# Kernel tuning notes

Hardware: AMD Instinct MI355X
Metric: run time of the kernel (lower is better)

The kernel has to match this reference:

```python
import jax, jax.numpy as jnp
from jax import lax
import numpy as np

INPUT_SIZE = 3
RESERVOIR = 2048
OUTPUT_SIZE = 3
SPECTRAL_RADIUS = 0.9
SPARSITY = 0.1
B, T = 16, 2048


def setup_inputs() -> dict:
    key = jax.random.key(0)
    kx, kwin, kw, kmask, kwo, kb = jax.random.split(key, 6)
    x = jax.random.normal(kx, (B, T, INPUT_SIZE), dtype=jnp.float32)
    Win = jax.random.normal(kwin, (RESERVOIR, INPUT_SIZE), dtype=jnp.float32)
    W = jax.random.normal(kw, (RESERVOIR, RESERVOIR), dtype=jnp.float32)
    # spectral-radius rescale (circular law: rho(randn(R,R)) ~ sqrt(R)), then sparsify
    W = W * (SPECTRAL_RADIUS / jnp.sqrt(jnp.float32(RESERVOIR)))
    mask = (jax.random.uniform(kmask, (RESERVOIR, RESERVOIR)) < SPARSITY).astype(jnp.float32)
    W = W * mask
    bound = 1.0 / np.sqrt(RESERVOIR)
    Wout_w = jax.random.uniform(kwo, (OUTPUT_SIZE, RESERVOIR), minval=-bound, maxval=bound, dtype=jnp.float32)
    Wout_b = jax.random.uniform(kb, (OUTPUT_SIZE,), minval=-bound, maxval=bound, dtype=jnp.float32)
    return {"x": x, "Win": Win, "W": W, "Wout_w": Wout_w, "Wout_b": Wout_b}


def reference(x, Win, W, Wout_w, Wout_b):
    Bsz = x.shape[0]
    R = W.shape[0]
    h0 = jnp.zeros((Bsz, R), dtype=x.dtype)

    def step(h, xt):
        h_new = jnp.tanh(xt @ Win.T + h @ W.T)  # [B, R]
        return h_new, h_new

    _, hs = lax.scan(step, h0, jnp.swapaxes(x, 0, 1))  # hs: [T, B, R]
    outs = hs @ Wout_w.T + Wout_b  # [T, B, O]
    return jnp.swapaxes(outs, 0, 1)  # [B, T, O]
```

## Files before the change

### kernel.cpp

```cpp
#include <hip/hip_runtime.h>
#include <math.h>


#define RDIM   2048
#define BATCH  16
#define TSTEPS 2048
#define NIN    3
#define NOUT   3
#define NBLK   256
#define NTHR   512

typedef unsigned u32x4 __attribute__((ext_vector_type(4)));

#define HT0_DW     0
#define HT1_DW     16384
#define WS_USED_DW 32768

#define POLL_MAX   (1L << 14)

#define TAGOK4(v, t) (((v)[0] >> 16) == (t) && ((v)[1] >> 16) == (t) && \
                      ((v)[2] >> 16) == (t) && ((v)[3] >> 16) == (t))

__device__ __forceinline__ void st1_uc(unsigned* p, unsigned v) {
    asm volatile("global_store_dword %0, %1, off sc0 sc1" :: "v"(p), "v"(v) : "memory");
}
__device__ __forceinline__ void pf_issue4(u32x4& v, const unsigned* p) {
    asm volatile("global_load_dwordx4 %0, %1, off sc0 sc1"
                 : "+v"(v) : "v"(p) : "memory");
}

__device__ __forceinline__ int q8(float v) {
    float c = fminf(127.f, fmaxf(-127.f, v));
    return (int)__builtin_rintf(c);
}
__device__ __forceinline__ unsigned pack4(int a, int b, int c, int d) {
    return (a & 0xff) | ((b & 0xff) << 8) | ((c & 0xff) << 16) | ((d & 0xff) << 24);
}
__device__ __forceinline__ int dot4i(unsigned a, unsigned b, int c) {
#if __has_builtin(__builtin_amdgcn_sdot4)
    return __builtin_amdgcn_sdot4((int)a, (int)b, c, false);
#else
    c += (int)(signed char)(a) * (int)(signed char)(b);
    c += (int)(signed char)(a >> 8)  * (int)(signed char)(b >> 8);
    c += (int)(signed char)(a >> 16) * (int)(signed char)(b >> 16);
    c += (int)(signed char)(a >> 24) * (int)(signed char)(b >> 24);
    return c;
#endif
}
__device__ __forceinline__ int dot16(uint4 wq, uint4 hq, int c) {
    c = dot4i(wq.x, hq.x, c);
    c = dot4i(wq.y, hq.y, c);
    c = dot4i(wq.z, hq.z, c);
    c = dot4i(wq.w, hq.w, c);
    return c;
}

extern "C" __global__ void __launch_bounds__(NTHR, 1) esn_persist(
    const float* __restrict__ W,
    const float* __restrict__ Win,
    const float* __restrict__ x,
    const float* __restrict__ Wout,
    const float* __restrict__ bout,
    unsigned* wsu,
    float* __restrict__ out)
{
    __shared__ int red[2][8][8][17];
    __shared__ __align__(16) unsigned hstage[2][2][512];
    __shared__ float wscale[64];
    extern __shared__ unsigned wlds[];

    const int tid  = threadIdx.x;
    const int lane = tid & 63;
    const int w    = tid >> 6;
    const int blk  = blockIdx.x;
    const int rg   = blk & 31;
    const int g    = blk >> 5;
    const int b0    = g * 2;
    const int kslot = lane >> 3;
    const int rgrp  = lane & 7;

#pragma unroll
    for (int rr = 0; rr < 8; ++rr) {
        const int   row = rg * 64 + w * 8 + rr;
        const float4* Wr = (const float4*)(W + (size_t)row * RDIM);
        float m = 0.f;
#pragma unroll
        for (int j = 0; j < 8; ++j) {
            float4 v = Wr[j * 64 + lane];
            m = fmaxf(m, fmaxf(fmaxf(fabsf(v.x), fabsf(v.y)),
                               fmaxf(fabsf(v.z), fabsf(v.w))));
        }
#pragma unroll
        for (int off = 32; off >= 1; off >>= 1)
            m = fmaxf(m, __shfl_xor(m, off, 64));
        const float inv = (m > 0.f) ? 127.f / m : 0.f;
        if (lane == 0) wscale[w * 8 + rr] = (m > 0.f) ? m / 127.f : 0.f;
#pragma unroll
        for (int j = 0; j < 8; ++j) {
            float4 v = Wr[j * 64 + lane];
            const int gsw = (j * 16 + (lane >> 2)) ^ w;
            wlds[(w * 8 + rr) * 512 + gsw * 4 + (lane & 3)] =
                pack4(q8(v.x * inv), q8(v.y * inv), q8(v.z * inv), q8(v.w * inv));
        }
    }

    float wn0 = 0.f, wn1 = 0.f, wn2 = 0.f;
    if (tid < 128) {
        const float* wp = Win + (size_t)(rg * 64 + (tid >> 1)) * NIN;
        wn0 = wp[0]; wn1 = wp[1]; wn2 = wp[2];
    }
    __syncthreads();

    unsigned* const ht0 = wsu + HT0_DW;
    unsigned* const ht1 = wsu + HT1_DW;

    const int woff = ((w << 6) + lane) << 2;

    u32x4 tv = {0, 0, 0, 0};
    pf_issue4(tv, ht0 + g * 2048 + woff);
    float xv0 = 0.f, xv1 = 0.f, xv2 = 0.f;
    if (tid < 128) {
        const float* xp = x + ((size_t)(b0 + (tid & 1)) * TSTEPS + 0) * NIN;
        xv0 = xp[0]; xv1 = xp[1]; xv2 = xp[2];
    }
    int dly = 6;

    for (int t = 0; t <= TSTEPS; ++t) {
        unsigned* const hb  = (t & 1) ? ht1 : ht0;
        unsigned* const hbn = (t & 1) ? ht0 : ht1;
        const unsigned tg  = (unsigned)t & 0xffffu;
        const unsigned tg1 = (unsigned)(t + 1) & 0xffffu;
        const int par = t & 1;

        bool first_hit;
        {
            const unsigned* p = hb + g * 2048 + woff;
            asm volatile("s_waitcnt vmcnt(0)" : "+v"(tv) :: "memory");
            bool ok = TAGOK4(tv, tg);
            first_hit = ok;
            long r = 0;
            while (!ok && r <= POLL_MAX) {
                ++r;
                if (r > 1) __builtin_amdgcn_s_sleep(2);
                asm volatile("global_load_dwordx4 %0, %1, off sc0 sc1\n\t"
                             "s_waitcnt vmcnt(0)"
                             : "+v"(tv) : "v"(p) : "memory");
                ok = TAGOK4(tv, tg);
            }
        }
        dly += __all((int)first_hit) ? -1 : 4;
        dly = dly < 0 ? 0 : (dly > 24 ? 24 : dly);

        const unsigned pdA = (tv[0] & 0xffffu) | (tv[1] << 16);
        const unsigned pdB = (tv[2] & 0xffffu) | (tv[3] << 16);
        hstage[par][0][(w << 6) + lane] = pdA;
        hstage[par][1][(w << 6) + lane] = pdB;

        if (t < TSTEPS) {
            const uint4* hwA = (const uint4*)&hstage[par][0][(w << 6) + (kslot << 3)];
            const uint4* hwB = (const uint4*)&hstage[par][1][(w << 6) + (kslot << 3)];
            const uint4 hA0 = hwA[0], hA1 = hwA[1];
            const uint4 hB0 = hwB[0], hB1 = hwB[1];

            int acc[8][2];
#pragma unroll
            for (int rr = 0; rr < 8; ++rr) { acc[rr][0] = 0; acc[rr][1] = 0; }
            const uint4* w4p = (const uint4*)wlds;
            const int g0 = (w << 4) + (((kslot << 1) ^ rgrp) & 15);
#pragma unroll
            for (int rr = 0; rr < 8; ++rr) {
                const int gi = (((rgrp << 3) + rr) << 7);
                uint4 w0 = w4p[gi + g0];
                uint4 w1 = w4p[gi + (g0 ^ 1)];
                acc[rr][0] = dot16(w0, hA0, acc[rr][0]);
                acc[rr][0] = dot16(w1, hA1, acc[rr][0]);
                acc[rr][1] = dot16(w0, hB0, acc[rr][1]);
                acc[rr][1] = dot16(w1, hB1, acc[rr][1]);
            }
#pragma unroll
            for (int rr = 0; rr < 8; ++rr)
#pragma unroll
                for (int b = 0; b < 2; ++b) {
                    int a = acc[rr][b];
                    a += __shfl_xor(a, 8, 64);
                    a += __shfl_xor(a, 16, 64);
                    a += __shfl_xor(a, 32, 64);
                    acc[rr][b] = a;
                }
            if (lane < 8) {
#pragma unroll
                for (int rr = 0; rr < 8; ++rr) {
                    red[par][w][lane][(rr << 1)]     = acc[rr][0];
                    red[par][w][lane][(rr << 1) + 1] = acc[rr][1];
                }
            }
        }
        __syncthreads();

        if (t < TSTEPS && tid < 128) {
            const int br = tid >> 1;
            const int b  = tid & 1;
            int s = 0;
#pragma unroll
            for (int wp = 0; wp < 8; ++wp)
                s += red[par][wp][br >> 3][((br & 7) << 1) + b];
            float pre = (float)s * wscale[br] * (1.f / 127.f)
                      + wn0 * xv0 + wn1 * xv1 + wn2 * xv2;
            const int qv = q8(tanhf(pre) * 127.f);
            const int qlo = __shfl(qv, ((lane >> 1) << 2) + (lane & 1), 64);
            const int qhi = __shfl(qv, ((lane >> 1) << 2) + 2 + (lane & 1), 64);
            if (lane < 32) {
                const int bb = lane & 1;
                const int u  = (w << 4) + (lane >> 1);
                unsigned dv = (unsigned)(qlo & 0xff) |
                              ((unsigned)(qhi & 0xff) << 8) | (tg1 << 16);
                st1_uc(hbn + g * 2048 + 64 * rg + ((u >> 1) << 2)
                           + (u & 1) + (bb << 1), dv);
            }
        }

        if (t + 1 < TSTEPS && tid < 128) {
            const float* xp = x + ((size_t)(b0 + (tid & 1)) * TSTEPS + (t + 1)) * NIN;
            xv0 = xp[0]; xv1 = xp[1]; xv2 = xp[2];
        }

        if (t < TSTEPS) {
            for (int i = 0; i < dly; ++i) __builtin_amdgcn_s_sleep(1);
            pf_issue4(tv, hbn + g * 2048 + woff);
        }

        if (t > 0 && rg == ((t - 1) & 31) && w >= 2) {
            const int pw = w - 2;
            const int b  = pw / NOUT;
            const int k  = pw % NOUT;
            const float4* wo4 = (const float4*)(Wout + (size_t)k * RDIM);
            float a = 0.f;
#pragma unroll
            for (int j = 0; j < 8; ++j) {
                unsigned hv = hstage[par][b][(lane << 3) + j];
                float4 wf = wo4[(lane << 3) + j];
                a += (float)(int)(signed char)(hv & 0xff)         * wf.x;
                a += (float)(int)(signed char)((hv >> 8) & 0xff)  * wf.y;
                a += (float)(int)(signed char)((hv >> 16) & 0xff) * wf.z;
                a += (float)(int)(signed char)(hv >> 24)          * wf.w;
            }
#pragma unroll
            for (int off = 32; off >= 1; off >>= 1)
                a += __shfl_xor(a, off, 64);
            if (lane == 0)
                out[((size_t)(b0 + b) * TSTEPS + (t - 1)) * NOUT + k] =
                    a * (1.f / 127.f) + bout[k];
        }
    }
}

extern "C" void kernel_launch(void* const* d_in, const int* in_sizes, int n_in,
                              void* d_out, int out_size, void* d_ws, size_t ws_size,
                              hipStream_t stream) {
    const float* x    = (const float*)d_in[0];
    const float* Win  = (const float*)d_in[1];
    const float* W    = (const float*)d_in[2];
    const float* Wout = (const float*)d_in[3];
    const float* bout = (const float*)d_in[4];
    float* out = (float*)d_out;
    unsigned* wsu = (unsigned*)d_ws;

    hipMemsetAsync(d_ws, 0, (size_t)WS_USED_DW * sizeof(unsigned), stream);

    hipFuncSetAttribute((const void*)esn_persist,
                        hipFuncAttributeMaxDynamicSharedMemorySize, 131072);

    void* args[] = {(void*)&W, (void*)&Win, (void*)&x, (void*)&Wout, (void*)&bout,
                    (void*)&wsu, (void*)&out};
    hipError_t e = hipLaunchCooperativeKernel((const void*)esn_persist,
                                              dim3(NBLK), dim3(NTHR),
                                              args, 131072, stream);
    if (e != hipSuccess) {
        esn_persist<<<dim3(NBLK), dim3(NTHR), 131072, stream>>>(
            W, Win, x, Wout, bout, wsu, out);
    }
}
```

Measured before the change: 6.114 ms.

## Keep quantized W slice in registers instead of LDS for recurrent matvec

Each thread now loads and quantizes its own 8x32 int8 slice of W once at startup and keeps it in 16 uint4 registers. The per-step recurrent dot products then read weights from registers instead of LDS. This removes 16 LDS uint4 loads per thread per step from the critical serial path. The output projection is also rewritten as a per-byte strided loop over hstage and Wout, and the cost is higher register pressure.

```diff
diff --git a/kernel.cpp b/kernel.cpp
--- a/kernel.cpp
+++ b/kernel.cpp
@@ -35,6 +35,9 @@
 }
 __device__ __forceinline__ unsigned pack4(int a, int b, int c, int d) {
     return (a & 0xff) | ((b & 0xff) << 8) | ((c & 0xff) << 16) | ((d & 0xff) << 24);
+}
+__device__ __forceinline__ unsigned qpack(float4 v, float inv) {
+    return pack4(q8(v.x * inv), q8(v.y * inv), q8(v.z * inv), q8(v.w * inv));
 }
 __device__ __forceinline__ int dot4i(unsigned a, unsigned b, int c) {
 #if __has_builtin(__builtin_amdgcn_sdot4)
@@ -67,7 +70,9 @@
     __shared__ int red[2][8][8][17];
     __shared__ __align__(16) unsigned hstage[2][2][512];
     __shared__ float wscale[64];
+    __shared__ float winv[64];
     extern __shared__ unsigned wlds[];
+    (void)wlds;
 
     const int tid  = threadIdx.x;
     const int lane = tid & 63;
@@ -93,15 +98,26 @@
 #pragma unroll
         for (int off = 32; off >= 1; off >>= 1)
             m = fmaxf(m, __shfl_xor(m, off, 64));
-        const float inv = (m > 0.f) ? 127.f / m : 0.f;
-        if (lane == 0) wscale[w * 8 + rr] = (m > 0.f) ? m / 127.f : 0.f;
-#pragma unroll
-        for (int j = 0; j < 8; ++j) {
-            float4 v = Wr[j * 64 + lane];
-            const int gsw = (j * 16 + (lane >> 2)) ^ w;
-            wlds[(w * 8 + rr) * 512 + gsw * 4 + (lane & 3)] =
-                pack4(q8(v.x * inv), q8(v.y * inv), q8(v.z * inv), q8(v.w * inv));
-        }
+        if (lane == 0) {
+            wscale[w * 8 + rr] = (m > 0.f) ? m / 127.f : 0.f;
+            winv[w * 8 + rr]   = (m > 0.f) ? 127.f / m : 0.f;
+        }
+    }
+    __syncthreads();
+
+    uint4 wr0[8], wr1[8];
+#pragma unroll
+    for (int rr = 0; rr < 8; ++rr) {
+        const int row = rg * 64 + 8 * rgrp + rr;
+        const float inv = winv[8 * rgrp + rr];
+        const float4* Wr = (const float4*)(W + (size_t)row * RDIM
+                                             + 256 * w + 32 * kslot);
+        float4 a0 = Wr[0], a1 = Wr[1], a2 = Wr[2], a3 = Wr[3];
+        float4 a4 = Wr[4], a5 = Wr[5], a6 = Wr[6], a7 = Wr[7];
+        wr0[rr] = make_uint4(qpack(a0, inv), qpack(a1, inv),
+                             qpack(a2, inv), qpack(a3, inv));
+        wr1[rr] = make_uint4(qpack(a4, inv), qpack(a5, inv),
+                             qpack(a6, inv), qpack(a7, inv));
     }
 
     float wn0 = 0.f, wn1 = 0.f, wn2 = 0.f;
@@ -109,7 +125,6 @@
         const float* wp = Win + (size_t)(rg * 64 + (tid >> 1)) * NIN;
         wn0 = wp[0]; wn1 = wp[1]; wn2 = wp[2];
     }
-    __syncthreads();
 
     unsigned* const ht0 = wsu + HT0_DW;
     unsigned* const ht1 = wsu + HT1_DW;
@@ -164,18 +179,13 @@
 
             int acc[8][2];
 #pragma unroll
-            for (int rr = 0; rr < 8; ++rr) { acc[rr][0] = 0; acc[rr][1] = 0; }
-            const uint4* w4p = (const uint4*)wlds;
-            const int g0 = (w << 4) + (((kslot << 1) ^ rgrp) & 15);
-#pragma unroll
             for (int rr = 0; rr < 8; ++rr) {
-                const int gi = (((rgrp << 3) + rr) << 7);
-                uint4 w0 = w4p[gi + g0];
-                uint4 w1 = w4p[gi + (g0 ^ 1)];
-                acc[rr][0] = dot16(w0, hA0, acc[rr][0]);
-                acc[rr][0] = dot16(w1, hA1, acc[rr][0]);
-                acc[rr][1] = dot16(w0, hB0, acc[rr][1]);
-                acc[rr][1] = dot16(w1, hB1, acc[rr][1]);
+                int a0 = dot16(wr0[rr], hA0, 0);
+                a0     = dot16(wr1[rr], hA1, a0);
+                int a1 = dot16(wr0[rr], hB0, 0);
+                a1     = dot16(wr1[rr], hB1, a1);
+                acc[rr][0] = a0;
+                acc[rr][1] = a1;
             }
 #pragma unroll
             for (int rr = 0; rr < 8; ++rr)
@@ -233,16 +243,12 @@
             const int pw = w - 2;
             const int b  = pw / NOUT;
             const int k  = pw % NOUT;
-            const float4* wo4 = (const float4*)(Wout + (size_t)k * RDIM);
+            const signed char* hsv = (const signed char*)hstage[par][b];
             float a = 0.f;
 #pragma unroll
-            for (int j = 0; j < 8; ++j) {
-                unsigned hv = hstage[par][b][(lane << 3) + j];
-                float4 wf = wo4[(lane << 3) + j];
-                a += (float)(int)(signed char)(hv & 0xff)         * wf.x;
-                a += (float)(int)(signed char)((hv >> 8) & 0xff)  * wf.y;
-                a += (float)(int)(signed char)((hv >> 16) & 0xff) * wf.z;
-                a += (float)(int)(signed char)(hv >> 24)          * wf.w;
+            for (int j = 0; j < 32; ++j) {
+                const int r = j * 64 + lane;
+                a += (float)hsv[r] * Wout[k * RDIM + r];
             }
 #pragma unroll
             for (int off = 32; off >= 1; off >>= 1)
```

After: 5.406 ms. -11.6%, faster.
